# Kernel optimization log

Hardware: AMD Instinct MI355X
Metric: run time of the kernel (lower is better)

## Reference

```python
import jax, jax.numpy as jnp
import numpy as np

D_MODEL = 1024
NUM_HEADS = 16
D_K = D_MODEL // NUM_HEADS
LN_EPS = 1e-5


def setup_inputs() -> dict:
    key = jax.random.key(0)
    ks = jax.random.split(key, 16)
    B, SQ, SK = 2, 2048, 2048
    s = 1.0 / np.sqrt(D_MODEL)
    inp = {
        "query": jax.random.normal(ks[0], (B, SQ, D_MODEL), jnp.float32),
        "key": jax.random.normal(ks[1], (B, SK, D_MODEL), jnp.float32),
        "value": jax.random.normal(ks[2], (B, SK, D_MODEL), jnp.float32),
        "mask": jax.random.randint(ks[3], (B, SQ, SK), 0, 2, jnp.int32),
        "w_q": jax.random.normal(ks[4], (D_MODEL, D_MODEL), jnp.float32) * s,
        "b_q": jnp.zeros((D_MODEL,), jnp.float32),
        "w_k": jax.random.normal(ks[5], (D_MODEL, D_MODEL), jnp.float32) * s,
        "b_k": jnp.zeros((D_MODEL,), jnp.float32),
        "w_v": jax.random.normal(ks[6], (D_MODEL, D_MODEL), jnp.float32) * s,
        "b_v": jnp.zeros((D_MODEL,), jnp.float32),
        "w_o": jax.random.normal(ks[7], (D_MODEL, D_MODEL), jnp.float32) * s,
        "b_o": jnp.zeros((D_MODEL,), jnp.float32),
        "ln_gamma": jnp.ones((D_MODEL,), jnp.float32),
        "ln_beta": jnp.zeros((D_MODEL,), jnp.float32),
    }
    return inp


def _split_heads(x):
    B, S, _ = x.shape
    return x.reshape(B, S, NUM_HEADS, D_K).transpose(0, 2, 1, 3)  # [B,H,S,Dk]


def reference(query, key, value, mask, w_q, b_q, w_k, b_k, w_v, b_v, w_o, b_o, ln_gamma, ln_beta):
    residual = query
    # torch Linear: y = x @ W.T + b
    Q = _split_heads(jnp.einsum('bsd,ed->bse', query, w_q) + b_q)
    K = _split_heads(jnp.einsum('bsd,ed->bse', key, w_k) + b_k)
    V = _split_heads(jnp.einsum('bsd,ed->bse', value, w_v) + b_v)
    scores = jnp.einsum('bhqd,bhkd->bhqk', Q, K) / jnp.sqrt(jnp.float32(D_K))
    scores = jnp.where(mask[:, None, :, :] == 0, jnp.float32(-1e9), scores)
    attn = jax.nn.softmax(scores, axis=-1)
    # dropout: eval mode (identity)
    ctx = jnp.einsum('bhqk,bhkd->bhqd', attn, V)
    B, H, SQ, Dk = ctx.shape
    ctx = ctx.transpose(0, 2, 1, 3).reshape(B, SQ, D_MODEL)
    out = jnp.einsum('bsd,ed->bse', ctx, w_o) + b_o + residual
    mu = jnp.mean(out, axis=-1, keepdims=True)
    var = jnp.mean(jnp.square(out - mu), axis=-1, keepdims=True)
    out = (out - mu) * jax.lax.rsqrt(var + LN_EPS) * ln_gamma + ln_beta
    return out
```

## Files before the change

kernel.cpp:

```cpp
#include <hip/hip_runtime.h>

typedef unsigned short u16;
typedef __attribute__((ext_vector_type(8))) short bf16x8;
typedef __attribute__((ext_vector_type(4))) float f32x4;

#define LOG2E 1.4426950408889634f
#define QSCALE (LOG2E / 8.0f)
#define PSTR 72

__device__ __forceinline__ u16 f2bf(float f) {
  union { float f; unsigned u; } v; v.f = f;
  unsigned r = v.u + 0x7fffu + ((v.u >> 16) & 1u);
  return (u16)(r >> 16);
}

__device__ __forceinline__ void gload_lds16(const void* g, void* l) {
  __builtin_amdgcn_global_load_lds(
      (const __attribute__((address_space(1))) unsigned int*)(unsigned long long)g,
      (__attribute__((address_space(3))) unsigned int*)(unsigned int)(unsigned long long)l,
      16, 0, 0);
}

__global__ __launch_bounds__(256) void prep_kernel(
    const float* __restrict__ q, const float* __restrict__ k, const float* __restrict__ v,
    const float* __restrict__ wq, const float* __restrict__ wk, const float* __restrict__ wv,
    const float* __restrict__ wo, const int* __restrict__ mask,
    u16* __restrict__ Xq, u16* __restrict__ Xk, u16* __restrict__ Xv,
    u16* __restrict__ Wq, u16* __restrict__ Wk, u16* __restrict__ Wv, u16* __restrict__ Wo,
    unsigned long long* __restrict__ Mp) {
  const int bx = blockIdx.x;
  if (bx < 16384) {
    const float* src; u16* dst; float sc; int idx;
    if (bx < 12288) {
      int seg = bx >> 12;
      idx = (bx & 4095) * 256 + threadIdx.x;
      src = seg == 0 ? q : (seg == 1 ? k : v);
      dst = seg == 0 ? Xq : (seg == 1 ? Xk : Xv);
      sc = 1.f;
    } else {
      int t = bx - 12288, seg = t >> 10;
      idx = (t & 1023) * 256 + threadIdx.x;
      src = seg == 0 ? wq : (seg == 1 ? wk : (seg == 2 ? wv : wo));
      dst = seg == 0 ? Wq : (seg == 1 ? Wk : (seg == 2 ? Wv : Wo));
      sc = seg == 0 ? QSCALE : 1.f;
    }
    float4 x = ((const float4*)src)[idx];
    ushort4 o;
    o.x = f2bf(x.x * sc); o.y = f2bf(x.y * sc);
    o.z = f2bf(x.z * sc); o.w = f2bf(x.w * sc);
    ((ushort4*)dst)[idx] = o;
  } else {
    int gw = (((bx - 16384) * 256) + threadIdx.x) >> 6;
    int lane = threadIdx.x & 63;
    for (int w = gw; w < 131072; w += 16384) {
      int m = mask[(size_t)w * 64 + lane];
      unsigned long long b = __ballot(m != 0);
      if (lane == 0) Mp[w] = b;
    }
  }
}

__global__ __launch_bounds__(256, 3) void gemm_kernel(
    const u16* __restrict__ Xq, const u16* __restrict__ Xk, const u16* __restrict__ Xv,
    const u16* __restrict__ Wq, const u16* __restrict__ Wk, const u16* __restrict__ Wv,
    const u16* __restrict__ Wo, const u16* __restrict__ Ctx,
    const float* __restrict__ bq, const float* __restrict__ bk, const float* __restrict__ bv,
    u16* __restrict__ Qd, u16* __restrict__ Kd, u16* __restrict__ Vtd, float* __restrict__ outp,
    int mode_base) {
  __shared__ __align__(16) u16 SH[17408];
  u16* As = SH;
  u16* Bs = SH + 4096;
  const int mode = mode_base + blockIdx.z;
  const int tid = threadIdx.x;
  const int wid = tid >> 6, l = tid & 63, quad = l >> 4, ln = l & 15;
  const int wm = wid >> 1, wn = wid & 1;

  const u16 *A, *B; const float* bias;
  if (mode == 0)      { A = Wq; B = Xq;  bias = bq; }
  else if (mode == 1) { A = Wk; B = Xk;  bias = bk; }
  else if (mode == 2) { A = Xv; B = Wv;  bias = bv; }
  else                { A = Wo; B = Ctx; bias = bq; }
  int mBase, nBase;
  if (mode == 2) { mBase = blockIdx.x * 128; nBase = blockIdx.y * 128; }
  else           { mBase = blockIdx.y * 128; nBase = blockIdx.x * 128; }

  const u16* Ag = A + (size_t)mBase * 1024;
  const u16* Bg = B + (size_t)nBase * 1024;

  f32x4 acc[4][4] = {};

  for (int k0 = 0; k0 < 1024; k0 += 32) {
    if (k0) __syncthreads();
    {
      int i0 = tid, i1 = tid + 256;
      gload_lds16(Ag + (size_t)(i0 & 127) * 1024 + k0 + (i0 >> 7) * 8, &As[i0 * 8]);
      gload_lds16(Ag + (size_t)(i1 & 127) * 1024 + k0 + (i1 >> 7) * 8, &As[i1 * 8]);
      gload_lds16(Bg + (size_t)(i0 & 127) * 1024 + k0 + (i0 >> 7) * 8, &Bs[i0 * 8]);
      gload_lds16(Bg + (size_t)(i1 & 127) * 1024 + k0 + (i1 >> 7) * 8, &Bs[i1 * 8]);
    }
    __syncthreads();
    bf16x8 af[4], bf[4];
#pragma unroll
    for (int i = 0; i < 4; ++i)
      af[i] = *(const bf16x8*)&As[(quad * 128 + wm * 64 + i * 16 + ln) * 8];
#pragma unroll
    for (int j = 0; j < 4; ++j)
      bf[j] = *(const bf16x8*)&Bs[(quad * 128 + wn * 64 + j * 16 + ln) * 8];
#pragma unroll
    for (int i = 0; i < 4; ++i)
#pragma unroll
      for (int j = 0; j < 4; ++j)
        acc[i][j] = __builtin_amdgcn_mfma_f32_16x16x32_bf16(af[i], bf[j], acc[i][j], 0, 0, 0);
  }

  __syncthreads();

  if (mode <= 1) {
    const float bscale = (mode == 0) ? QSCALE : 1.0f;
#pragma unroll
    for (int i = 0; i < 4; ++i) {
      int f0 = wm * 64 + i * 16 + quad * 4;
      float4 bb = *(const float4*)(bias + mBase + f0);
#pragma unroll
      for (int j = 0; j < 4; ++j) {
        int sl = wn * 64 + j * 16 + ln;
        f32x4 v = acc[i][j];
        ushort4 o;
        o.x = f2bf(v[0] + bb.x * bscale); o.y = f2bf(v[1] + bb.y * bscale);
        o.z = f2bf(v[2] + bb.z * bscale); o.w = f2bf(v[3] + bb.w * bscale);
        *(ushort4*)&SH[sl * 136 + f0] = o;
      }
    }
    __syncthreads();
    u16* dstQK = (mode == 0) ? Qd : Kd;
#pragma unroll
    for (int p = 0; p < 8; ++p) {
      int sl = p * 16 + (tid >> 4);
      int fl = (tid & 15) * 8;
      uint4 w = *(const uint4*)&SH[sl * 136 + fl];
      int s = nBase + sl, f = mBase + fl;
      int h = f >> 6, d = f & 63, b = s >> 11, sr = s & 2047;
      *(uint4*)(dstQK + (((size_t)(b * 16 + h) * 2048 + sr) * 64 + d)) = w;
    }
  } else if (mode == 2) {
#pragma unroll
    for (int j = 0; j < 4; ++j) {
      int fl = wn * 64 + j * 16 + ln;
      float bb = bias[nBase + fl];
#pragma unroll
      for (int i = 0; i < 4; ++i) {
        int s0 = wm * 64 + i * 16 + quad * 4;
        f32x4 v = acc[i][j];
        ushort4 o;
        o.x = f2bf(v[0] + bb); o.y = f2bf(v[1] + bb);
        o.z = f2bf(v[2] + bb); o.w = f2bf(v[3] + bb);
        *(ushort4*)&SH[fl * 136 + s0] = o;
      }
    }
    __syncthreads();
#pragma unroll
    for (int p = 0; p < 8; ++p) {
      int fl = p * 16 + (tid >> 4);
      int sl = (tid & 15) * 8;
      uint4 w = *(const uint4*)&SH[fl * 136 + sl];
      int f = nBase + fl, s = mBase + sl;
      int h = f >> 6, d = f & 63, b = s >> 11, sr = s & 2047;
      *(uint4*)(Vtd + (((size_t)(b * 16 + h) * 64 + d) * 2048 + sr)) = w;
    }
  } else {
    float* ES = (float*)SH;
#pragma unroll
    for (int h2 = 0; h2 < 2; ++h2) {
      if (h2) __syncthreads();
      if (wn == h2) {
#pragma unroll
        for (int i = 0; i < 4; ++i) {
          int f0 = wm * 64 + i * 16 + quad * 4;
#pragma unroll
          for (int j = 0; j < 4; ++j) {
            int sl = j * 16 + ln;
            f32x4 v = acc[i][j];
            float4 o; o.x = v[0]; o.y = v[1]; o.z = v[2]; o.w = v[3];
            *(float4*)&ES[sl * 132 + f0] = o;
          }
        }
      }
      __syncthreads();
#pragma unroll
      for (int p = 0; p < 8; ++p) {
        int sl = p * 8 + (tid >> 5);
        int fl = (tid & 31) * 4;
        float4 w = *(const float4*)&ES[sl * 132 + fl];
        int s = nBase + h2 * 64 + sl;
        *(float4*)(outp + (size_t)s * 1024 + mBase + fl) = w;
      }
    }
  }
}

__global__ __launch_bounds__(256, 3) void attn_kernel(
    const u16* __restrict__ Qg, const u16* __restrict__ Kg, const u16* __restrict__ Vtg,
    const unsigned* __restrict__ Mp, u16* __restrict__ ctx) {
  __shared__ __align__(16) u16 Ks[8192];
  __shared__ __align__(16) u16 Vs[8192];
  __shared__ __align__(16) u16 Ps[9216];
  const int tid = threadIdx.x;
  const int wid = tid >> 6, l = tid & 63, quad = l >> 4, ln = l & 15;
  const int q4 = quad * 4;
  const int L = blockIdx.x;
  const int bh = (L & 7) + 8 * (L >> 7);
  const int b = bh >> 4, h = bh & 15;
  const int qBase = ((L >> 3) & 15) * 128;
  const int wq = wid * 32;

  bf16x8 qf[2][2];
#pragma unroll
  for (int qt = 0; qt < 2; ++qt)
#pragma unroll
    for (int kc = 0; kc < 2; ++kc)
      qf[qt][kc] = *(const bf16x8*)(Qg + (((size_t)bh * 2048 + qBase + wq + qt * 16 + ln) * 64 +
                                          kc * 32 + quad * 8));

  f32x4 oacc[2][4] = {};
  f32x4 lsum[2] = {};
  const bf16x8 vone = {(short)0x3F80, (short)0x3F80, (short)0x3F80, (short)0x3F80,
                       (short)0x3F80, (short)0x3F80, (short)0x3F80, (short)0x3F80};

  const unsigned* mrow[2];
  mrow[0] = Mp + ((size_t)b * 2048 + qBase + wq + ln) * 64;
  mrow[1] = mrow[0] + 16 * 64;

  for (int it = 0; it < 16; ++it) {
    const int kvB = it * 128;
    __syncthreads();
#pragma unroll
    for (int r = 0; r < 4; ++r) {
      int c = r * 256 + tid;
      gload_lds16(Kg + (((size_t)bh * 2048 + kvB + (c & 127)) * 64 + (c >> 7) * 8), &Ks[c * 8]);
    }
#pragma unroll
    for (int r = 0; r < 4; ++r) {
      int c = r * 256 + tid;
      gload_lds16(Vtg + (((size_t)bh * 64 + (c & 63)) * 2048 + kvB + (c >> 6) * 8), &Vs[c * 8]);
    }
    __syncthreads();

    unsigned ww[2][4];
    {
      uint4 m0 = *(const uint4*)(mrow[0] + it * 4);
      uint4 m1 = *(const uint4*)(mrow[1] + it * 4);
      ww[0][0] = m0.x; ww[0][1] = m0.y; ww[0][2] = m0.z; ww[0][3] = m0.w;
      ww[1][0] = m1.x; ww[1][1] = m1.y; ww[1][2] = m1.z; ww[1][3] = m1.w;
    }

#pragma unroll
    for (int hf = 0; hf < 2; ++hf) {
      f32x4 s[4][2];
#pragma unroll
      for (int m2 = 0; m2 < 4; ++m2) {
        int mt = hf * 4 + m2;
        bf16x8 k0 = *(const bf16x8*)&Ks[((0 + quad) * 128 + mt * 16 + ln) * 8];
        bf16x8 k1 = *(const bf16x8*)&Ks[((4 + quad) * 128 + mt * 16 + ln) * 8];
#pragma unroll
        for (int qt = 0; qt < 2; ++qt) {
          f32x4 z = {0.f, 0.f, 0.f, 0.f};
          z = __builtin_amdgcn_mfma_f32_16x16x32_bf16(k0, qf[qt][0], z, 0, 0, 0);
          s[m2][qt] = __builtin_amdgcn_mfma_f32_16x16x32_bf16(k1, qf[qt][1], z, 0, 0, 0);
        }
      }

      uint2 pk[4][2];
#pragma unroll
      for (int qt = 0; qt < 2; ++qt)
#pragma unroll
        for (int m2 = 0; m2 < 4; ++m2) {
          int mt = hf * 4 + m2;
          unsigned nib = (ww[qt][mt >> 1] >> ((mt & 1) * 16 + q4)) & 0xFu;
          float p0 = __builtin_amdgcn_exp2f((nib & 1u) ? s[m2][qt][0] : -1e30f);
          float p1 = __builtin_amdgcn_exp2f((nib & 2u) ? s[m2][qt][1] : -1e30f);
          float p2 = __builtin_amdgcn_exp2f((nib & 4u) ? s[m2][qt][2] : -1e30f);
          float p3 = __builtin_amdgcn_exp2f((nib & 8u) ? s[m2][qt][3] : -1e30f);
          pk[m2][qt].x = __builtin_amdgcn_perm(__float_as_uint(p1) + 0x8000u,
                                               __float_as_uint(p0) + 0x8000u, 0x07060302u);
          pk[m2][qt].y = __builtin_amdgcn_perm(__float_as_uint(p3) + 0x8000u,
                                               __float_as_uint(p2) + 0x8000u, 0x07060302u);
        }

#pragma unroll
      for (int qt = 0; qt < 2; ++qt) {
        int qrow = wq + qt * 16 + ln;
#pragma unroll
        for (int m2 = 0; m2 < 4; ++m2)
          *(uint2*)&Ps[qrow * PSTR + m2 * 16 + q4] = pk[m2][qt];
      }

#pragma unroll
      for (int k2 = 0; k2 < 2; ++k2) {
        int kc2 = hf * 2 + k2;
        bf16x8 aP[2];
#pragma unroll
        for (int qt = 0; qt < 2; ++qt)
          aP[qt] = *(const bf16x8*)&Ps[(wq + qt * 16 + ln) * PSTR + k2 * 32 + quad * 8];
#pragma unroll
        for (int nt = 0; nt < 4; ++nt) {
          bf16x8 bV = *(const bf16x8*)&Vs[((kc2 * 4 + quad) * 64 + nt * 16 + ln) * 8];
#pragma unroll
          for (int qt = 0; qt < 2; ++qt)
            oacc[qt][nt] = __builtin_amdgcn_mfma_f32_16x16x32_bf16(aP[qt], bV, oacc[qt][nt], 0, 0, 0);
        }
#pragma unroll
        for (int qt = 0; qt < 2; ++qt)
          lsum[qt] = __builtin_amdgcn_mfma_f32_16x16x32_bf16(aP[qt], vone, lsum[qt], 0, 0, 0);
      }
    }
  }

  __syncthreads();
#pragma unroll
  for (int qt = 0; qt < 2; ++qt)
#pragma unroll
    for (int r = 0; r < 4; ++r) {
      float il = 1.0f / lsum[qt][r];
      int q = wq + qt * 16 + q4 + r;
#pragma unroll
      for (int nt = 0; nt < 4; ++nt)
        Ps[q * 64 + nt * 16 + ln] = f2bf(oacc[qt][nt][r] * il);
    }
  __syncthreads();
#pragma unroll
  for (int r = 0; r < 4; ++r) {
    int c = r * 256 + tid;
    int q = c >> 3, ch = c & 7;
    *(uint4*)(ctx + ((size_t)(b * 2048 + qBase + q) * 1024 + h * 64 + ch * 8)) =
        *(const uint4*)&Ps[q * 64 + ch * 8];
  }
}

__global__ __launch_bounds__(256) void ln_kernel(const float* __restrict__ x,
                                                 const float* __restrict__ resid,
                                                 const float* __restrict__ bo,
                                                 const float* __restrict__ gamma,
                                                 const float* __restrict__ beta,
                                                 float* __restrict__ out) {
  __shared__ float red[8];
  const int tid = threadIdx.x;
  const size_t row = blockIdx.x;
  float4 v = ((const float4*)(x + row * 1024))[tid];
  const float4 rr = ((const float4*)(resid + row * 1024))[tid];
  const float4 bb = ((const float4*)bo)[tid];
  v.x += rr.x + bb.x; v.y += rr.y + bb.y; v.z += rr.z + bb.z; v.w += rr.w + bb.w;
  float s1 = v.x + v.y + v.z + v.w;
  float s2 = v.x * v.x + v.y * v.y + v.z * v.z + v.w * v.w;
#pragma unroll
  for (int o = 32; o >= 1; o >>= 1) {
    s1 += __shfl_xor(s1, o);
    s2 += __shfl_xor(s2, o);
  }
  if ((tid & 63) == 0) { red[(tid >> 6) * 2] = s1; red[(tid >> 6) * 2 + 1] = s2; }
  __syncthreads();
  s1 = red[0] + red[2] + red[4] + red[6];
  s2 = red[1] + red[3] + red[5] + red[7];
  float mu = s1 * (1.f / 1024.f);
  float var = s2 * (1.f / 1024.f) - mu * mu;
  float inv = rsqrtf(var + 1e-5f);
  float4 g = ((const float4*)gamma)[tid];
  float4 be = ((const float4*)beta)[tid];
  float4 o;
  o.x = (v.x - mu) * inv * g.x + be.x;
  o.y = (v.y - mu) * inv * g.y + be.y;
  o.z = (v.z - mu) * inv * g.z + be.z;
  o.w = (v.w - mu) * inv * g.w + be.w;
  ((float4*)(out + row * 1024))[tid] = o;
}

extern "C" void kernel_launch(void* const* d_in, const int* in_sizes, int n_in,
                              void* d_out, int out_size, void* d_ws, size_t ws_size,
                              hipStream_t stream) {
  const float* query = (const float*)d_in[0];
  const float* key   = (const float*)d_in[1];
  const float* value = (const float*)d_in[2];
  const int*   mask  = (const int*)d_in[3];
  const float* w_q = (const float*)d_in[4];
  const float* b_q = (const float*)d_in[5];
  const float* w_k = (const float*)d_in[6];
  const float* b_k = (const float*)d_in[7];
  const float* w_v = (const float*)d_in[8];
  const float* b_v = (const float*)d_in[9];
  const float* w_o = (const float*)d_in[10];
  const float* b_o = (const float*)d_in[11];
  const float* ln_g = (const float*)d_in[12];
  const float* ln_b = (const float*)d_in[13];
  float* out = (float*)d_out;

  char* ws = (char*)d_ws;
  u16* Xq = (u16*)(ws + ((size_t)0 << 20));
  u16* Xk = (u16*)(ws + ((size_t)8 << 20));
  u16* Xv = (u16*)(ws + ((size_t)16 << 20));
  float* outpre = (float*)(ws + ((size_t)8 << 20));
  u16* Wq = (u16*)(ws + ((size_t)24 << 20));
  u16* Wk = (u16*)(ws + ((size_t)26 << 20));
  u16* Wv = (u16*)(ws + ((size_t)28 << 20));
  u16* Wo = (u16*)(ws + ((size_t)30 << 20));
  u16* Qd = (u16*)(ws + ((size_t)32 << 20));
  u16* Kd = (u16*)(ws + ((size_t)40 << 20));
  u16* Vtd = (u16*)(ws + ((size_t)48 << 20));
  unsigned long long* Mp = (unsigned long long*)(ws + ((size_t)56 << 20));
  u16* ctx = Xq;

  prep_kernel<<<20480, 256, 0, stream>>>(query, key, value, w_q, w_k, w_v, w_o, mask,
                                         Xq, Xk, Xv, Wq, Wk, Wv, Wo, Mp);
  gemm_kernel<<<dim3(32, 8, 3), 256, 0, stream>>>(Xq, Xk, Xv, Wq, Wk, Wv, Wo, ctx,
      b_q, b_k, b_v, Qd, Kd, Vtd, outpre, 0);
  attn_kernel<<<dim3(512), 256, 0, stream>>>(Qd, Kd, Vtd, (const unsigned*)Mp, ctx);
  gemm_kernel<<<dim3(32, 8, 1), 256, 0, stream>>>(Xq, Xk, Xv, Wq, Wk, Wv, Wo, ctx,
      b_q, b_k, b_v, Qd, Kd, Vtd, outpre, 3);
  ln_kernel<<<4096, 256, 0, stream>>>(outpre, query, b_o, ln_g, ln_b, out);
}
```

Baseline: 318.9 us.

## Double-buffer K/V tiles in attention kernel and XOR-swizzle P buffer

The attention kernel now keeps two K/V LDS buffers and issues the async global-to-LDS loads for the next tile before computing on the current one. This hides load latency and removes one barrier per tile. The padded P stride is replaced with an XOR swizzle to avoid bank conflicts while shrinking P storage. The larger LDS footprint lowers the occupancy target from 3 to 2 blocks per CU, which reduces latency hiding across blocks.

```diff
diff --git a/kernel.cpp b/kernel.cpp
--- a/kernel.cpp
+++ b/kernel.cpp
@@ -6,7 +6,6 @@
 
 #define LOG2E 1.4426950408889634f
 #define QSCALE (LOG2E / 8.0f)
-#define PSTR 72
 
 __device__ __forceinline__ u16 f2bf(float f) {
   union { float f; unsigned u; } v; v.f = f;
@@ -198,12 +197,14 @@
   }
 }
 
-__global__ __launch_bounds__(256, 3) void attn_kernel(
+__global__ __launch_bounds__(256, 2) void attn_kernel(
     const u16* __restrict__ Qg, const u16* __restrict__ Kg, const u16* __restrict__ Vtg,
     const unsigned* __restrict__ Mp, u16* __restrict__ ctx) {
-  __shared__ __align__(16) u16 Ks[8192];
-  __shared__ __align__(16) u16 Vs[8192];
-  __shared__ __align__(16) u16 Ps[9216];
+  __shared__ __align__(16) u16 Ks0[8192];
+  __shared__ __align__(16) u16 Ks1[8192];
+  __shared__ __align__(16) u16 Vs0[8192];
+  __shared__ __align__(16) u16 Vs1[8192];
+  __shared__ __align__(16) u16 Ps[8192];
   const int tid = threadIdx.x;
   const int wid = tid >> 6, l = tid & 63, quad = l >> 4, ln = l & 15;
   const int q4 = quad * 4;
@@ -212,6 +213,7 @@
   const int b = bh >> 4, h = bh & 15;
   const int qBase = ((L >> 3) & 15) * 128;
   const int wq = wid * 32;
+  const int sw = (ln & 7) << 3;
 
   bf16x8 qf[2][2];
 #pragma unroll
@@ -230,90 +232,103 @@
   mrow[0] = Mp + ((size_t)b * 2048 + qBase + wq + ln) * 64;
   mrow[1] = mrow[0] + 16 * 64;
 
-  for (int it = 0; it < 16; ++it) {
-    const int kvB = it * 128;
+  const u16* KgB = Kg + (size_t)bh * 2048 * 64;
+  const u16* VgB = Vtg + (size_t)bh * 64 * 2048;
+
+#define STAGE_TILE(KS, VS, t_)                                                  \
+  do {                                                                          \
+    const int kvB_ = (t_) * 128;                                                \
+    _Pragma("unroll")                                                           \
+    for (int r_ = 0; r_ < 4; ++r_) {                                            \
+      int c_ = r_ * 256 + tid;                                                  \
+      gload_lds16(KgB + (size_t)(kvB_ + (c_ & 127)) * 64 + (c_ >> 7) * 8,       \
+                  &KS[c_ * 8]);                                                 \
+      gload_lds16(VgB + (size_t)(c_ & 63) * 2048 + kvB_ + (c_ >> 6) * 8,        \
+                  &VS[c_ * 8]);                                                 \
+    }                                                                           \
+  } while (0)
+
+#define COMPUTE_TILE(KS, VS, it_)                                                         \
+  do {                                                                                    \
+    unsigned ww[2][4];                                                                    \
+    {                                                                                     \
+      uint4 m0 = *(const uint4*)(mrow[0] + (it_) * 4);                                    \
+      uint4 m1 = *(const uint4*)(mrow[1] + (it_) * 4);                                    \
+      ww[0][0] = m0.x; ww[0][1] = m0.y; ww[0][2] = m0.z; ww[0][3] = m0.w;                 \
+      ww[1][0] = m1.x; ww[1][1] = m1.y; ww[1][2] = m1.z; ww[1][3] = m1.w;                 \
+    }                                                                                     \
+    _Pragma("unroll")                                                                     \
+    for (int hf = 0; hf < 2; ++hf) {                                                      \
+      f32x4 s[4][2];                                                                      \
+      _Pragma("unroll")                                                                   \
+      for (int m2 = 0; m2 < 4; ++m2) {                                                    \
+        int mt = hf * 4 + m2;                                                             \
+        bf16x8 k0 = *(const bf16x8*)&KS[((0 + quad) * 128 + mt * 16 + ln) * 8];           \
+        bf16x8 k1 = *(const bf16x8*)&KS[((4 + quad) * 128 + mt * 16 + ln) * 8];           \
+        _Pragma("unroll")                                                                 \
+        for (int qt = 0; qt < 2; ++qt) {                                                  \
+          f32x4 z = {0.f, 0.f, 0.f, 0.f};                                                 \
+          z = __builtin_amdgcn_mfma_f32_16x16x32_bf16(k0, qf[qt][0], z, 0, 0, 0);         \
+          s[m2][qt] = __builtin_amdgcn_mfma_f32_16x16x32_bf16(k1, qf[qt][1], z, 0, 0, 0); \
+        }                                                                                 \
+      }                                                                                   \
+      uint2 pk[4][2];                                                                     \
+      _Pragma("unroll")                                                                   \
+      for (int qt = 0; qt < 2; ++qt)                                                      \
+        _Pragma("unroll")                                                                 \
+        for (int m2 = 0; m2 < 4; ++m2) {                                                  \
+          int mt = hf * 4 + m2;                                                           \
+          unsigned nib = (ww[qt][mt >> 1] >> ((mt & 1) * 16 + q4)) & 0xFu;                \
+          float p0 = __builtin_amdgcn_exp2f((nib & 1u) ? s[m2][qt][0] : -1e30f);          \
+          float p1 = __builtin_amdgcn_exp2f((nib & 2u) ? s[m2][qt][1] : -1e30f);          \
+          float p2 = __builtin_amdgcn_exp2f((nib & 4u) ? s[m2][qt][2] : -1e30f);          \
+          float p3 = __builtin_amdgcn_exp2f((nib & 8u) ? s[m2][qt][3] : -1e30f);          \
+          pk[m2][qt].x = __builtin_amdgcn_perm(__float_as_uint(p1) + 0x8000u,             \
+                                               __float_as_uint(p0) + 0x8000u, 0x07060302u); \
+          pk[m2][qt].y = __builtin_amdgcn_perm(__float_as_uint(p3) + 0x8000u,             \
+                                               __float_as_uint(p2) + 0x8000u, 0x07060302u); \
+        }                                                                                 \
+              \
+      _Pragma("unroll")                                                                   \
+      for (int qt = 0; qt < 2; ++qt) {                                                    \
+        int qrow = wq + qt * 16 + ln;                                                     \
+        _Pragma("unroll")                                                                 \
+        for (int m2 = 0; m2 < 4; ++m2)                                                    \
+          *(uint2*)&Ps[(qrow * 64 + m2 * 16 + q4) ^ sw] = pk[m2][qt];                     \
+      }                                                                                   \
+      _Pragma("unroll")                                                                   \
+      for (int k2 = 0; k2 < 2; ++k2) {                                                    \
+        int kc2 = hf * 2 + k2;                                                            \
+        bf16x8 aP[2];                                                                     \
+        _Pragma("unroll")                                                                 \
+        for (int qt = 0; qt < 2; ++qt)                                                    \
+          aP[qt] = *(const bf16x8*)&Ps[((wq + qt * 16 + ln) * 64 + k2 * 32 + quad * 8) ^ sw]; \
+        _Pragma("unroll")                                                                 \
+        for (int nt = 0; nt < 4; ++nt) {                                                  \
+          bf16x8 bV = *(const bf16x8*)&VS[((kc2 * 4 + quad) * 64 + nt * 16 + ln) * 8];    \
+          _Pragma("unroll")                                                               \
+          for (int qt = 0; qt < 2; ++qt)                                                  \
+            oacc[qt][nt] = __builtin_amdgcn_mfma_f32_16x16x32_bf16(aP[qt], bV, oacc[qt][nt], 0, 0, 0); \
+        }                                                                                 \
+        _Pragma("unroll")                                                                 \
+        for (int qt = 0; qt < 2; ++qt)                                                    \
+          lsum[qt] = __builtin_amdgcn_mfma_f32_16x16x32_bf16(aP[qt], vone, lsum[qt], 0, 0, 0); \
+      }                                                                                   \
+    }                                                                                     \
+  } while (0)
+
+  STAGE_TILE(Ks0, Vs0, 0);
+#pragma unroll 1
+  for (int it2 = 0; it2 < 8; ++it2) {
     __syncthreads();
-#pragma unroll
-    for (int r = 0; r < 4; ++r) {
-      int c = r * 256 + tid;
-      gload_lds16(Kg + (((size_t)bh * 2048 + kvB + (c & 127)) * 64 + (c >> 7) * 8), &Ks[c * 8]);
-    }
-#pragma unroll
-    for (int r = 0; r < 4; ++r) {
-      int c = r * 256 + tid;
-      gload_lds16(Vtg + (((size_t)bh * 64 + (c & 63)) * 2048 + kvB + (c >> 6) * 8), &Vs[c * 8]);
-    }
+    STAGE_TILE(Ks1, Vs1, 2 * it2 + 1);
+    COMPUTE_TILE(Ks0, Vs0, 2 * it2);
     __syncthreads();
-
-    unsigned ww[2][4];
-    {
-      uint4 m0 = *(const uint4*)(mrow[0] + it * 4);
-      uint4 m1 = *(const uint4*)(mrow[1] + it * 4);
-      ww[0][0] = m0.x; ww[0][1] = m0.y; ww[0][2] = m0.z; ww[0][3] = m0.w;
-      ww[1][0] = m1.x; ww[1][1] = m1.y; ww[1][2] = m1.z; ww[1][3] = m1.w;
-    }
-
-#pragma unroll
-    for (int hf = 0; hf < 2; ++hf) {
-      f32x4 s[4][2];
-#pragma unroll
-      for (int m2 = 0; m2 < 4; ++m2) {
-        int mt = hf * 4 + m2;
-        bf16x8 k0 = *(const bf16x8*)&Ks[((0 + quad) * 128 + mt * 16 + ln) * 8];
-        bf16x8 k1 = *(const bf16x8*)&Ks[((4 + quad) * 128 + mt * 16 + ln) * 8];
-#pragma unroll
-        for (int qt = 0; qt < 2; ++qt) {
-          f32x4 z = {0.f, 0.f, 0.f, 0.f};
-          z = __builtin_amdgcn_mfma_f32_16x16x32_bf16(k0, qf[qt][0], z, 0, 0, 0);
-          s[m2][qt] = __builtin_amdgcn_mfma_f32_16x16x32_bf16(k1, qf[qt][1], z, 0, 0, 0);
-        }
-      }
-
-      uint2 pk[4][2];
-#pragma unroll
-      for (int qt = 0; qt < 2; ++qt)
-#pragma unroll
-        for (int m2 = 0; m2 < 4; ++m2) {
-          int mt = hf * 4 + m2;
-          unsigned nib = (ww[qt][mt >> 1] >> ((mt & 1) * 16 + q4)) & 0xFu;
-          float p0 = __builtin_amdgcn_exp2f((nib & 1u) ? s[m2][qt][0] : -1e30f);
-          float p1 = __builtin_amdgcn_exp2f((nib & 2u) ? s[m2][qt][1] : -1e30f);
-          float p2 = __builtin_amdgcn_exp2f((nib & 4u) ? s[m2][qt][2] : -1e30f);
-          float p3 = __builtin_amdgcn_exp2f((nib & 8u) ? s[m2][qt][3] : -1e30f);
-          pk[m2][qt].x = __builtin_amdgcn_perm(__float_as_uint(p1) + 0x8000u,
-                                               __float_as_uint(p0) + 0x8000u, 0x07060302u);
-          pk[m2][qt].y = __builtin_amdgcn_perm(__float_as_uint(p3) + 0x8000u,
-                                               __float_as_uint(p2) + 0x8000u, 0x07060302u);
-        }
-
-#pragma unroll
-      for (int qt = 0; qt < 2; ++qt) {
-        int qrow = wq + qt * 16 + ln;
-#pragma unroll
-        for (int m2 = 0; m2 < 4; ++m2)
-          *(uint2*)&Ps[qrow * PSTR + m2 * 16 + q4] = pk[m2][qt];
-      }
-
-#pragma unroll
-      for (int k2 = 0; k2 < 2; ++k2) {
-        int kc2 = hf * 2 + k2;
-        bf16x8 aP[2];
-#pragma unroll
-        for (int qt = 0; qt < 2; ++qt)
-          aP[qt] = *(const bf16x8*)&Ps[(wq + qt * 16 + ln) * PSTR + k2 * 32 + quad * 8];
-#pragma unroll
-        for (int nt = 0; nt < 4; ++nt) {
-          bf16x8 bV = *(const bf16x8*)&Vs[((kc2 * 4 + quad) * 64 + nt * 16 + ln) * 8];
-#pragma unroll
-          for (int qt = 0; qt < 2; ++qt)
-            oacc[qt][nt] = __builtin_amdgcn_mfma_f32_16x16x32_bf16(aP[qt], bV, oacc[qt][nt], 0, 0, 0);
-        }
-#pragma unroll
-        for (int qt = 0; qt < 2; ++qt)
-          lsum[qt] = __builtin_amdgcn_mfma_f32_16x16x32_bf16(aP[qt], vone, lsum[qt], 0, 0, 0);
-      }
-    }
-  }
+    if (it2 < 7) STAGE_TILE(Ks0, Vs0, 2 * it2 + 2);
+    COMPUTE_TILE(Ks1, Vs1, 2 * it2 + 1);
+  }
+#undef STAGE_TILE
+#undef COMPUTE_TILE
 
   __syncthreads();
 #pragma unroll
```

Result: no change. 316.6 us (-0.7%).
